# Performance work log

Measured on AMD Instinct MI355X. Metric: run time of the kernel, lower is better.

Reference implementation:

```python
import jax, jax.numpy as jnp
import numpy as np

N, E, ND, ED, H, OUT, L, VC = 10000, 160000, 8, 4, 128, 256, 6, 6
HEADS, C = 4, 128  # GATConv: out_channels=128 per head, concat=False -> mean over heads


def _ln(x, g, b, eps=1e-5):
    m = x.mean(-1, keepdims=True)
    v = ((x - m) ** 2).mean(-1, keepdims=True)
    return (x - m) * jax.lax.rsqrt(v + eps) * g + b


def _gat_layer(h, src, dst, e_attr, lw, a_src, a_dst, lew, a_edge, bias):
    # h: [N,H]; e_attr: [Etot,H]; PyG GATConv(heads=4, concat=False, edge_dim=H)
    xh = (h @ lw).reshape(N, HEADS, C)                 # [N,4,128]
    eh = (e_attr @ lew).reshape(-1, HEADS, C)          # [Etot,4,128]
    al_s = jnp.einsum('nhc,hc->nh', xh, a_src)
    al_d = jnp.einsum('nhc,hc->nh', xh, a_dst)
    al_e = jnp.einsum('ehc,hc->eh', eh, a_edge)
    alpha = jax.nn.leaky_relu(al_s[src] + al_d[dst] + al_e, 0.2)  # [Etot,4]
    amax = jax.ops.segment_max(alpha, dst, num_segments=N)
    ex = jnp.exp(alpha - amax[dst])
    den = jax.ops.segment_sum(ex, dst, num_segments=N)
    w = ex / (den[dst] + 1e-16)
    out = jax.ops.segment_sum(xh[src] * w[..., None], dst, num_segments=N)  # [N,4,128]
    return out.mean(axis=1) + bias


def setup_inputs() -> dict:
    key = jax.random.key(0)
    ks = jax.random.split(key, 32)
    s = 0.05
    d = {
        'x': jax.random.normal(ks[0], (N, ND), jnp.float32),
        'edge_index': jax.random.randint(ks[1], (2, E), 0, N),
        'edge_attr': jax.random.uniform(ks[2], (E, ED), jnp.float32),
        'vnf_context': jax.random.normal(ks[3], (1, VC), jnp.float32),
        # node embedding
        'node_w': jax.random.normal(ks[4], (ND, H)) * s, 'node_b': jnp.zeros((H,)),
        # EdgeAttentionLayer
        'ea_proj_w': jax.random.normal(ks[5], (ED, H)) * s, 'ea_proj_b': jnp.zeros((H,)),
        'vnf_w': jax.random.normal(ks[6], (VC, H)) * s, 'vnf_b': jnp.zeros((H,)),
        'att1_w': jax.random.normal(ks[7], (2 * H, H)) * s, 'att1_b': jnp.zeros((H,)),
        'att2_w': jax.random.normal(ks[8], (H, H // 2)) * s, 'att2_b': jnp.zeros((H // 2,)),
        'att3_w': jax.random.normal(ks[9], (H // 2, 1)) * s, 'att3_b': jnp.zeros((1,)),
        # per-layer GATConv params (stacked over L layers)
        'gat_lin_w': jax.random.normal(ks[10], (L, H, HEADS * C)) * s,
        'gat_att_src': jax.random.normal(ks[11], (L, HEADS, C)) * s,
        'gat_att_dst': jax.random.normal(ks[12], (L, HEADS, C)) * s,
        'gat_lin_edge_w': jax.random.normal(ks[13], (L, H, HEADS * C)) * s,
        'gat_att_edge': jax.random.normal(ks[14], (L, HEADS, C)) * s,
        'gat_bias': jnp.zeros((L, C)),
        'ln_scale': jnp.ones((L, H)), 'ln_bias': jnp.zeros((L, H)),
        # output projection
        'out_w': jax.random.normal(ks[15], (H, OUT)) * s, 'out_b': jnp.zeros((OUT,)),
    }
    return d


def reference(x, edge_index, edge_attr, vnf_context, node_w, node_b, ea_proj_w, ea_proj_b,
              vnf_w, vnf_b, att1_w, att1_b, att2_w, att2_b, att3_w, att3_b,
              gat_lin_w, gat_att_src, gat_att_dst, gat_lin_edge_w, gat_att_edge, gat_bias,
              ln_scale, ln_bias, out_w, out_b):
    src, dst = edge_index[0], edge_index[1]
    h = x @ node_w + node_b                                   # [N,128]
    # EdgeAttentionLayer (eval mode, no network_state)
    ef = edge_attr @ ea_proj_w + ea_proj_b                    # [E,128]
    vnf = vnf_context @ vnf_w + vnf_b                         # [1,128]
    comb = jnp.concatenate([ef, jnp.broadcast_to(vnf, (E, H))], axis=-1)
    a = jax.nn.relu(comb @ att1_w + att1_b)
    a = jax.nn.relu(a @ att2_w + att2_b)
    e_gate = jax.nn.sigmoid(a @ att3_w + att3_b)              # [E,1]
    w_edge = ef * e_gate                                      # [E,128]
    # GATConv default add_self_loops=True, fill_value='mean'
    loop = jnp.arange(N)
    src2 = jnp.concatenate([src, loop])
    dst2 = jnp.concatenate([dst, loop])
    e2 = jnp.concatenate([w_edge, jnp.broadcast_to(w_edge.mean(0, keepdims=True), (N, H))], axis=0)
    for l in range(L):
        hc = _gat_layer(h, src2, dst2, e2, gat_lin_w[l], gat_att_src[l], gat_att_dst[l],
                        gat_lin_edge_w[l], gat_att_edge[l], gat_bias[l])
        h = _ln(h + jax.nn.relu(hc), ln_scale[l], ln_bias[l])
    return h @ out_w + out_b                                  # [N,256]
```

## Files before the change

### kernel.cpp

```cpp
#include <hip/hip_runtime.h>
#include <hip/hip_bf16.h>
#include <math.h>

#define Nn 10000
#define Ee 160000
#define ET 170000
#define LL 6

typedef short v8s __attribute__((ext_vector_type(8)));
typedef float v4f __attribute__((ext_vector_type(4)));
typedef float v2f __attribute__((ext_vector_type(2)));

__device__ __forceinline__ unsigned short f2bf(float v) {
    unsigned int b = __float_as_uint(v);
    b += 0x7fffu + ((b >> 16) & 1u);
    return (unsigned short)(b >> 16);
}
__device__ __forceinline__ float bflo(unsigned int u) { return __uint_as_float(u << 16); }
__device__ __forceinline__ float bfhi(unsigned int u) { return __uint_as_float(u & 0xffff0000u); }

__global__ void k_node_embed(const float* __restrict__ x, const float* __restrict__ nw,
                             const float* __restrict__ nb, float* __restrict__ h,
                             unsigned short* __restrict__ hb) {
    int idx = blockIdx.x * 256 + threadIdx.x;
    if (idx >= Nn * 128) return;
    int n = idx >> 7, c = idx & 127;
    const float* xr = x + (size_t)n * 8;
    float acc = nb[c];
#pragma unroll
    for (int k = 0; k < 8; k++) acc += xr[k] * nw[k * 128 + c];
    h[idx] = acc;
    hb[idx] = f2bf(acc);
}

__global__ void k_small(const float* __restrict__ vnfc, const float* __restrict__ vw,
                        const float* __restrict__ vb, const float* __restrict__ eab,
                        const float* __restrict__ a1w, const float* __restrict__ a1b,
                        const float* __restrict__ eaw, float* __restrict__ E1) {
    __shared__ float vr[128];
    __shared__ float sM1[512];
    __shared__ float sd1[128];
    int t = threadIdx.x;
    if (t < 128) {
        float a = vb[t];
#pragma unroll
        for (int k = 0; k < 6; k++) a += vnfc[k] * vw[k * 128 + t];
        vr[t] = a;
    }
    __syncthreads();
    if (t < 128) {
        float a = a1b[t];
        for (int k = 0; k < 128; k++) a += eab[k] * a1w[k * 128 + t];
        for (int k = 0; k < 128; k++) a += vr[k] * a1w[(128 + k) * 128 + t];
        sd1[t] = a;
    }
    {
        int r = t >> 7, j = t & 127;
        float a = 0.f;
        for (int k = 0; k < 128; k++) a += eaw[r * 128 + k] * a1w[k * 128 + j];
        sM1[r * 128 + j] = a;
    }
    __syncthreads();
    if (t < 128) {
        E1[t * 8 + 0] = sM1[t];
        E1[t * 8 + 1] = sM1[128 + t];
        E1[t * 8 + 2] = sM1[256 + t];
        E1[t * 8 + 3] = sM1[384 + t];
        E1[t * 8 + 4] = sd1[t];
        E1[t * 8 + 5] = 0.f; E1[t * 8 + 6] = 0.f; E1[t * 8 + 7] = 0.f;
    }
}

__global__ void k_bmat(const float* __restrict__ glw, const float* __restrict__ gas,
                       const float* __restrict__ gad, const float* __restrict__ glew,
                       const float* __restrict__ gae, float* __restrict__ Bs,
                       float* __restrict__ Bd, float* __restrict__ Be) {
    int idx = blockIdx.x * 256 + threadIdx.x;
    if (idx >= LL * 128 * 4) return;
    int hh = idx & 3, k = (idx >> 2) & 127, l = idx >> 9;
    const float* lwp = glw  + (size_t)l * 65536 + k * 512 + hh * 128;
    const float* lep = glew + (size_t)l * 65536 + k * 512 + hh * 128;
    const float* sp = gas + l * 512 + hh * 128;
    const float* dp = gad + l * 512 + hh * 128;
    const float* ep = gae + l * 512 + hh * 128;
    float s1 = 0, s2 = 0, s3 = 0;
    for (int c = 0; c < 128; c++) {
        float lv = lwp[c];
        s1 += lv * sp[c];
        s2 += lv * dp[c];
        s3 += lep[c] * ep[c];
    }
    Bs[idx] = s1; Bd[idx] = s2; Be[idx] = s3;
}

__global__ void k_wsum(const float* __restrict__ glw, unsigned short* __restrict__ WsumT) {
    int idx = blockIdx.x * 256 + threadIdx.x;
    if (idx >= LL * 128 * 512) return;
    int kk = idx & 511;
    int c = (idx >> 9) & 127;
    int l = idx >> 16;
    float v = 0.25f * glw[(size_t)l * 65536 + (size_t)(kk & 127) * 512 + (kk >> 7) * 128 + c];
    WsumT[(size_t)l * 65536 + (size_t)c * 512 + kk] = f2bf(v);
}

__global__ void k_pb(const float* __restrict__ eaw, const float* __restrict__ eab,
                     const float* __restrict__ Be, float* __restrict__ PB,
                     float* __restrict__ cB) {
    int t = threadIdx.x;
    if (t >= 24) return;
    int l = t >> 2, hh = t & 3;
    const float* bp = Be + l * 512 + hh;
    float s0 = 0, s1 = 0, s2 = 0, s3 = 0, sc = 0;
    for (int k = 0; k < 128; k++) {
        float bv = bp[k * 4];
        s0 += eaw[0 * 128 + k] * bv;
        s1 += eaw[1 * 128 + k] * bv;
        s2 += eaw[2 * 128 + k] * bv;
        s3 += eaw[3 * 128 + k] * bv;
        sc += eab[k] * bv;
    }
    PB[0 * 24 + t] = s0; PB[1 * 24 + t] = s1;
    PB[2 * 24 + t] = s2; PB[3 * 24 + t] = s3;
    cB[t] = sc;
}

__global__ __launch_bounds__(256, 3) void k_edge(
    const float* __restrict__ ea, const float* __restrict__ E1,
    const float* __restrict__ a2w, const float* __restrict__ a2b,
    const float* __restrict__ a3w, const float* __restrict__ a3b,
    float* __restrict__ Gg, float4* __restrict__ Ge4, float* __restrict__ gsum) {
    __shared__ float sw2[128 * 64];
    __shared__ float4 sM[128];
    __shared__ float sD[128];
    __shared__ float prs[4][256];
    __shared__ float gsh[256];
    int t = threadIdx.x;
    int lane = t & 63;
    int p = t >> 6;
    int ps = __builtin_amdgcn_readfirstlane(p);
    for (int z = t; z < 2048; z += 256) ((float4*)sw2)[z] = ((const float4*)a2w)[z];
    if (t < 128) { sM[t] = *(const float4*)(E1 + t * 8); sD[t] = E1[t * 8 + 4]; }
    __syncthreads();
    int eb = blockIdx.x * 256 + lane;
    float4 ev[4];
#pragma unroll
    for (int r = 0; r < 4; r++) ev[r] = *(const float4*)(ea + (size_t)(eb + r * 64) * 4);
    v2f acc[4][8];
#pragma unroll
    for (int j = 0; j < 8; j++) {
        v2f b = {a2b[ps * 16 + 2 * j], a2b[ps * 16 + 2 * j + 1]};
#pragma unroll
        for (int r = 0; r < 4; r++) acc[r][j] = b;
    }
    const float* w2base = sw2 + ps * 16;
    for (int k = 0; k < 128; k++) {
        float4 m = sM[k];
        float dk = sD[k];
        v2f xx[4];
#pragma unroll
        for (int r = 0; r < 4; r++) {
            float xv = fmaxf(dk + ev[r].x * m.x + ev[r].y * m.y + ev[r].z * m.z + ev[r].w * m.w, 0.f);
            xx[r][0] = xv; xx[r][1] = xv;
        }
        const float* w2r = w2base + k * 64;
#pragma unroll
        for (int j4 = 0; j4 < 4; j4++) {
            float4 wv = *(const float4*)(w2r + j4 * 4);
            v2f w01 = {wv.x, wv.y}, w23 = {wv.z, wv.w};
#pragma unroll
            for (int r = 0; r < 4; r++) {
                acc[r][2 * j4]     += xx[r] * w01;
                acc[r][2 * j4 + 1] += xx[r] * w23;
            }
        }
    }
#pragma unroll
    for (int r = 0; r < 4; r++) {
        float pr = 0.f;
#pragma unroll
        for (int j = 0; j < 8; j++) {
            pr += fmaxf(acc[r][j][0], 0.f) * a3w[ps * 16 + 2 * j];
            pr += fmaxf(acc[r][j][1], 0.f) * a3w[ps * 16 + 2 * j + 1];
        }
        prs[p][r * 64 + lane] = pr;
    }
    __syncthreads();
    if (p == 0) {
        float v0 = 0.f, v1 = 0.f, v2 = 0.f, v3 = 0.f, v4 = 0.f;
#pragma unroll
        for (int rep = 0; rep < 4; rep++) {
            int le = rep * 64 + lane;
            float tot = prs[0][le] + prs[1][le] + prs[2][le] + prs[3][le] + a3b[0];
            float g = 1.f / (1.f + __expf(-tot));
            gsh[le] = g;
            float4 evv = ev[rep];
            v0 += g; v1 += g * evv.x; v2 += g * evv.y; v3 += g * evv.z; v4 += g * evv.w;
        }
#pragma unroll
        for (int d = 32; d > 0; d >>= 1) {
            v0 += __shfl_down(v0, d); v1 += __shfl_down(v1, d); v2 += __shfl_down(v2, d);
            v3 += __shfl_down(v3, d); v4 += __shfl_down(v4, d);
        }
        if (lane == 0) {
            atomicAdd(&gsum[0], v0); atomicAdd(&gsum[1], v1); atomicAdd(&gsum[2], v2);
            atomicAdd(&gsum[3], v3); atomicAdd(&gsum[4], v4);
        }
    }
    __syncthreads();
    {
        int e = blockIdx.x * 256 + ps * 64 + lane;
        float g = gsh[ps * 64 + lane];
        float4 evv = *(const float4*)(ea + (size_t)e * 4);
        Gg[e] = g;
        Ge4[e] = make_float4(g * evv.x, g * evv.y, g * evv.z, g * evv.w);
    }
}

__global__ void k_hist(const int* __restrict__ ei, int* __restrict__ hist) {
    int i = blockIdx.x * 256 + threadIdx.x;
    if (i >= ET) return;
    int d = (i < Ee) ? ei[Ee + i] : (i - Ee);
    atomicAdd(&hist[d], 1);
}

__global__ __launch_bounds__(1024) void k_scan(const int* __restrict__ hist,
                                               int* __restrict__ seg, int* __restrict__ pos) {
    __shared__ int wsums[16];
    __shared__ int carry_s;
    int t = threadIdx.x;
    int lane = t & 63, wid = t >> 6;
    if (t == 0) { carry_s = 0; seg[0] = 0; }
    __syncthreads();
    for (int base = 0; base < Nn; base += 1024) {
        int idx = base + t;
        int v = (idx < Nn) ? hist[idx] : 0;
        int sc = v;
#pragma unroll
        for (int d = 1; d < 64; d <<= 1) {
            int up = __shfl_up(sc, d);
            if (lane >= d) sc += up;
        }
        if (lane == 63) wsums[wid] = sc;
        __syncthreads();
        if (wid == 0) {
            int wv = (lane < 16) ? wsums[lane] : 0;
            int wsc = wv;
#pragma unroll
            for (int d = 1; d < 16; d <<= 1) {
                int up = __shfl_up(wsc, d);
                if (lane >= d) wsc += up;
            }
            if (lane < 16) wsums[lane] = wsc - wv;
        }
        __syncthreads();
        int carry = carry_s;
        int inc = sc + wsums[wid] + carry;
        if (idx < Nn) { seg[idx + 1] = inc; pos[idx] = inc - v; }
        __syncthreads();
        if (t == 1023) carry_s = inc;
        __syncthreads();
    }
}

__global__ void k_scatter(const int* __restrict__ ei, int* __restrict__ pos,
                          int2* __restrict__ pse) {
    int i = blockIdx.x * 256 + threadIdx.x;
    if (i >= ET) return;
    int s, d;
    if (i < Ee) { s = ei[i]; d = ei[Ee + i]; } else { s = d = i - Ee; }
    int idx = atomicAdd(&pos[d], 1);
    pse[idx] = make_int2(s, i);
}

__global__ void k_ales(const int2* __restrict__ pse, const float* __restrict__ Gg,
                       const float4* __restrict__ Ge4, const float* __restrict__ gsum,
                       const float* __restrict__ PB, const float* __restrict__ cB,
                       float4* __restrict__ aleS) {
    int i = blockIdx.x * 256 + threadIdx.x;
    if (i >= ET) return;
    int y = pse[i].y;
    float g;
    float4 ge;
    if (y < Ee) { g = Gg[y]; ge = Ge4[y]; }
    else {
        float inv = 1.f / Ee;
        g = gsum[0] * inv;
        ge = make_float4(gsum[1] * inv, gsum[2] * inv, gsum[3] * inv, gsum[4] * inv);
    }
#pragma unroll
    for (int l = 0; l < LL; l++) {
        float4 o;
        o.x = g * cB[l * 4 + 0] + ge.x * PB[0 * 24 + l * 4 + 0] + ge.y * PB[1 * 24 + l * 4 + 0]
            + ge.z * PB[2 * 24 + l * 4 + 0] + ge.w * PB[3 * 24 + l * 4 + 0];
        o.y = g * cB[l * 4 + 1] + ge.x * PB[0 * 24 + l * 4 + 1] + ge.y * PB[1 * 24 + l * 4 + 1]
            + ge.z * PB[2 * 24 + l * 4 + 1] + ge.w * PB[3 * 24 + l * 4 + 1];
        o.z = g * cB[l * 4 + 2] + ge.x * PB[0 * 24 + l * 4 + 2] + ge.y * PB[1 * 24 + l * 4 + 2]
            + ge.z * PB[2 * 24 + l * 4 + 2] + ge.w * PB[3 * 24 + l * 4 + 2];
        o.w = g * cB[l * 4 + 3] + ge.x * PB[0 * 24 + l * 4 + 3] + ge.y * PB[1 * 24 + l * 4 + 3]
            + ge.z * PB[2 * 24 + l * 4 + 3] + ge.w * PB[3 * 24 + l * 4 + 3];
        aleS[(size_t)l * ET + i] = o;
    }
}

__global__ void k_ab(const float* __restrict__ h, const float* __restrict__ Bs_l,
                     const float* __restrict__ Bd_l, float* __restrict__ als,
                     float* __restrict__ ald) {
    int idx = blockIdx.x * 256 + threadIdx.x;
    if (idx >= Nn * 8) return;
    int n = idx >> 3, slot = idx & 7;
    const float* B = (slot < 4) ? Bs_l : Bd_l;
    int hh = slot & 3;
    const float4* hr = (const float4*)(h + (size_t)n * 128);
    float s = 0.f;
#pragma unroll 8
    for (int kb = 0; kb < 32; kb++) {
        float4 hv = hr[kb];
        s += hv.x * B[(4 * kb + 0) * 4 + hh] + hv.y * B[(4 * kb + 1) * 4 + hh]
           + hv.z * B[(4 * kb + 2) * 4 + hh] + hv.w * B[(4 * kb + 3) * 4 + hh];
    }
    if (slot < 4) als[n * 4 + hh] = s;
    else          ald[n * 4 + hh] = s;
}

__global__ __launch_bounds__(256) void k_agg4(
    const int2* __restrict__ pse, const int* __restrict__ seg,
    const float* __restrict__ als, const float* __restrict__ ald,
    const float4* __restrict__ aleS_l, const unsigned short* __restrict__ hb,
    unsigned short* __restrict__ aggb) {
    __shared__ float part[3][512];
    __shared__ float pden[3][4];
    int t = threadIdx.x;
    int lane = t & 63;
    int wv = t >> 6;
    int n = blockIdx.x;
    int start = seg[n], end = seg[n + 1];
    int deg = end - start;
    int quarter = (deg + 3) >> 2;
    int s0 = start + wv * quarter;
    int e0 = min(s0 + quarter, end);
    int hp = lane >> 4;
    int cch = (lane & 15) * 8;
    float aldh = ald[n * 4 + hp];
    float den = 0.f;
    float4 acc0 = make_float4(0.f, 0.f, 0.f, 0.f);
    float4 acc1 = make_float4(0.f, 0.f, 0.f, 0.f);
    int i = s0;
    for (; i + 2 <= e0; i += 2) {
        int sa = pse[i].x, sb = pse[i + 1].x;
        float4 ala4 = aleS_l[i], alb4 = aleS_l[i + 1];
        float ala = hp == 0 ? ala4.x : hp == 1 ? ala4.y : hp == 2 ? ala4.z : ala4.w;
        float alb = hp == 0 ? alb4.x : hp == 1 ? alb4.y : hp == 2 ? alb4.z : alb4.w;
        float ava = als[sa * 4 + hp] + aldh + ala;
        float avb = als[sb * 4 + hp] + aldh + alb;
        ava = ava > 0.f ? ava : 0.2f * ava;
        avb = avb > 0.f ? avb : 0.2f * avb;
        float ea = __expf(fminf(ava, 60.f));
        float eb = __expf(fminf(avb, 60.f));
        den += ea + eb;
        uint4 ua = *(const uint4*)(hb + (size_t)sa * 128 + cch);
        uint4 ub = *(const uint4*)(hb + (size_t)sb * 128 + cch);
        acc0.x += ea * bflo(ua.x) + eb * bflo(ub.x);
        acc0.y += ea * bfhi(ua.x) + eb * bfhi(ub.x);
        acc0.z += ea * bflo(ua.y) + eb * bflo(ub.y);
        acc0.w += ea * bfhi(ua.y) + eb * bfhi(ub.y);
        acc1.x += ea * bflo(ua.z) + eb * bflo(ub.z);
        acc1.y += ea * bfhi(ua.z) + eb * bfhi(ub.z);
        acc1.z += ea * bflo(ua.w) + eb * bflo(ub.w);
        acc1.w += ea * bfhi(ua.w) + eb * bfhi(ub.w);
    }
    if (i < e0) {
        int sa = pse[i].x;
        float4 ala4 = aleS_l[i];
        float ala = hp == 0 ? ala4.x : hp == 1 ? ala4.y : hp == 2 ? ala4.z : ala4.w;
        float ava = als[sa * 4 + hp] + aldh + ala;
        ava = ava > 0.f ? ava : 0.2f * ava;
        float ea = __expf(fminf(ava, 60.f));
        den += ea;
        uint4 ua = *(const uint4*)(hb + (size_t)sa * 128 + cch);
        acc0.x += ea * bflo(ua.x); acc0.y += ea * bfhi(ua.x);
        acc0.z += ea * bflo(ua.y); acc0.w += ea * bfhi(ua.y);
        acc1.x += ea * bflo(ua.z); acc1.y += ea * bfhi(ua.z);
        acc1.z += ea * bflo(ua.w); acc1.w += ea * bfhi(ua.w);
    }
    if (wv > 0) {
        *(float4*)&part[wv - 1][lane * 8] = acc0;
        *(float4*)&part[wv - 1][lane * 8 + 4] = acc1;
        if ((lane & 15) == 0) pden[wv - 1][hp] = den;
    }
    __syncthreads();
    if (wv == 0) {
        float dtot = den + pden[0][hp] + pden[1][hp] + pden[2][hp];
#pragma unroll
        for (int r = 0; r < 3; r++) {
            float4 p0 = *(const float4*)&part[r][lane * 8];
            float4 p1 = *(const float4*)&part[r][lane * 8 + 4];
            acc0.x += p0.x; acc0.y += p0.y; acc0.z += p0.z; acc0.w += p0.w;
            acc1.x += p1.x; acc1.y += p1.y; acc1.z += p1.z; acc1.w += p1.w;
        }
        float inv = 1.f / (dtot + 1e-16f);
        acc0.x *= inv; acc0.y *= inv; acc0.z *= inv; acc0.w *= inv;
        acc1.x *= inv; acc1.y *= inv; acc1.z *= inv; acc1.w *= inv;
        ushort4 q0, q1;
        q0.x = f2bf(acc0.x); q0.y = f2bf(acc0.y); q0.z = f2bf(acc0.z); q0.w = f2bf(acc0.w);
        q1.x = f2bf(acc1.x); q1.y = f2bf(acc1.y); q1.z = f2bf(acc1.z); q1.w = f2bf(acc1.w);
        *(ushort4*)(aggb + (size_t)n * 512 + lane * 8) = q0;
        *(ushort4*)(aggb + (size_t)n * 512 + lane * 8 + 4) = q1;
    }
}

__global__ __launch_bounds__(256) void k_post(
    const unsigned short* __restrict__ aggb, const unsigned short* __restrict__ WsumT_l,
    const float* __restrict__ gbias, const float* __restrict__ lnsc,
    const float* __restrict__ lnbi, float* __restrict__ h,
    unsigned short* __restrict__ hb, const float* __restrict__ Bs_n,
    const float* __restrict__ Bd_n, float* __restrict__ als, float* __restrict__ ald) {
    int t = threadIdx.x;
    int lane = t & 63, w = t >> 6;
    int n0 = (blockIdx.x * 4 + w) * 16;
    if (n0 >= Nn) return;
    int m = lane & 15, q = lane >> 4;
    v4f acc[8];
#pragma unroll
    for (int nt = 0; nt < 8; nt++) acc[nt] = (v4f){0.f, 0.f, 0.f, 0.f};
    const unsigned short* arow = aggb + (size_t)(n0 + m) * 512 + q * 8;
#pragma unroll 4
    for (int ks = 0; ks < 16; ks++) {
        v8s fa = *(const v8s*)(arow + ks * 32);
#pragma unroll
        for (int nt = 0; nt < 8; nt++) {
            int col = nt * 16 + m;
            v8s fb = *(const v8s*)(WsumT_l + (size_t)col * 512 + ks * 32 + q * 8);
            acc[nt] = __builtin_amdgcn_mfma_f32_16x16x32_bf16(fa, fb, acc[nt], 0, 0, 0);
        }
    }
    float v[8][4];
    float s1[4] = {0.f, 0.f, 0.f, 0.f}, s2[4] = {0.f, 0.f, 0.f, 0.f};
#pragma unroll
    for (int nt = 0; nt < 8; nt++) {
        int col = nt * 16 + m;
        float b = gbias[col];
#pragma unroll
        for (int r = 0; r < 4; r++) {
            int row = n0 + q * 4 + r;
            float val = h[(size_t)row * 128 + col] + fmaxf(acc[nt][r] + b, 0.f);
            v[nt][r] = val;
            s1[r] += val; s2[r] += val * val;
        }
    }
#pragma unroll
    for (int d = 1; d <= 8; d <<= 1) {
#pragma unroll
        for (int r = 0; r < 4; r++) {
            s1[r] += __shfl_xor(s1[r], d);
            s2[r] += __shfl_xor(s2[r], d);
        }
    }
    float o8[8][4];
#pragma unroll
    for (int r = 0; r < 4; r++) {
        float mean = s1[r] * (1.f / 128.f);
        float var = s2[r] * (1.f / 128.f) - mean * mean;
        float rinv = rsqrtf(var + 1e-5f);
        int row = n0 + q * 4 + r;
#pragma unroll
        for (int nt = 0; nt < 8; nt++) {
            int col = nt * 16 + m;
            float o = (v[nt][r] - mean) * rinv * lnsc[col] + lnbi[col];
            o8[nt][r] = o;
            h[(size_t)row * 128 + col] = o;
            hb[(size_t)row * 128 + col] = f2bf(o);
        }
    }
    float sal[4][4], sad[4][4];
#pragma unroll
    for (int r = 0; r < 4; r++) {
#pragma unroll
        for (int hh = 0; hh < 4; hh++) { sal[r][hh] = 0.f; sad[r][hh] = 0.f; }
    }
#pragma unroll
    for (int nt = 0; nt < 8; nt++) {
        int col = nt * 16 + m;
        float4 bs = *(const float4*)(Bs_n + col * 4);
        float4 bd = *(const float4*)(Bd_n + col * 4);
#pragma unroll
        for (int r = 0; r < 4; r++) {
            float o = o8[nt][r];
            sal[r][0] += o * bs.x; sal[r][1] += o * bs.y;
            sal[r][2] += o * bs.z; sal[r][3] += o * bs.w;
            sad[r][0] += o * bd.x; sad[r][1] += o * bd.y;
            sad[r][2] += o * bd.z; sad[r][3] += o * bd.w;
        }
    }
#pragma unroll
    for (int d = 1; d <= 8; d <<= 1) {
#pragma unroll
        for (int r = 0; r < 4; r++) {
#pragma unroll
            for (int hh = 0; hh < 4; hh++) {
                sal[r][hh] += __shfl_xor(sal[r][hh], d);
                sad[r][hh] += __shfl_xor(sad[r][hh], d);
            }
        }
    }
    if (m < 8) {
        int hh = m & 3;
#pragma unroll
        for (int r = 0; r < 4; r++) {
            int row = n0 + q * 4 + r;
            float va = (hh == 0) ? sal[r][0] : (hh == 1) ? sal[r][1] : (hh == 2) ? sal[r][2] : sal[r][3];
            float vd = (hh == 0) ? sad[r][0] : (hh == 1) ? sad[r][1] : (hh == 2) ? sad[r][2] : sad[r][3];
            if (m < 4) als[row * 4 + hh] = va;
            else       ald[row * 4 + hh] = vd;
        }
    }
}

__global__ __launch_bounds__(256) void k_out(
    const float* __restrict__ h, const float* __restrict__ ow,
    const float* __restrict__ ob, float* __restrict__ out) {
    __shared__ float4 hs4[8][32];
    int t = threadIdx.x;
    int n0 = blockIdx.x * 8;
    if (t < 256) {
        int i = t >> 5, kb = t & 31;
        hs4[i][kb] = *(const float4*)(h + (size_t)(n0 + i) * 128 + 4 * kb);
    }
    __syncthreads();
    float acc[8] = {0, 0, 0, 0, 0, 0, 0, 0};
    for (int kb = 0; kb < 32; kb++) {
        float w0 = ow[(4 * kb + 0) * 256 + t];
        float w1 = ow[(4 * kb + 1) * 256 + t];
        float w2 = ow[(4 * kb + 2) * 256 + t];
        float w3 = ow[(4 * kb + 3) * 256 + t];
#pragma unroll
        for (int i = 0; i < 8; i++) {
            float4 hv = hs4[i][kb];
            acc[i] += hv.x * w0 + hv.y * w1 + hv.z * w2 + hv.w * w3;
        }
    }
    float b = ob[t];
#pragma unroll
    for (int i = 0; i < 8; i++) out[(size_t)(n0 + i) * 256 + t] = acc[i] + b;
}

extern "C" void kernel_launch(void* const* d_in, const int* in_sizes, int n_in,
                              void* d_out, int out_size, void* d_ws, size_t ws_size,
                              hipStream_t stream) {
    const float* x    = (const float*)d_in[0];
    const int*   ei   = (const int*)d_in[1];
    const float* ea   = (const float*)d_in[2];
    const float* vnfc = (const float*)d_in[3];
    const float* nw   = (const float*)d_in[4];
    const float* nb   = (const float*)d_in[5];
    const float* eaw  = (const float*)d_in[6];
    const float* eab  = (const float*)d_in[7];
    const float* vw   = (const float*)d_in[8];
    const float* vb   = (const float*)d_in[9];
    const float* a1w  = (const float*)d_in[10];
    const float* a1b  = (const float*)d_in[11];
    const float* a2w  = (const float*)d_in[12];
    const float* a2b  = (const float*)d_in[13];
    const float* a3w  = (const float*)d_in[14];
    const float* a3b  = (const float*)d_in[15];
    const float* glw  = (const float*)d_in[16];
    const float* gas  = (const float*)d_in[17];
    const float* gad  = (const float*)d_in[18];
    const float* glew = (const float*)d_in[19];
    const float* gae  = (const float*)d_in[20];
    const float* gb   = (const float*)d_in[21];
    const float* lnsc = (const float*)d_in[22];
    const float* lnbi = (const float*)d_in[23];
    const float* ow   = (const float*)d_in[24];
    const float* ob   = (const float*)d_in[25];
    float* out = (float*)d_out;

    char* w = (char*)d_ws;
    size_t o = 0;
    auto allocf = [&](size_t cnt) { float* p = (float*)(w + o); o += ((cnt * 4 + 255) / 256) * 256; return p; };
    auto alloci = [&](size_t cnt) { int* p = (int*)(w + o); o += ((cnt * 4 + 255) / 256) * 256; return p; };
    auto allocu = [&](size_t cnt) { unsigned short* p = (unsigned short*)(w + o); o += ((cnt * 2 + 255) / 256) * 256; return p; };
    float* h      = allocf((size_t)Nn * 128);
    unsigned short* hb    = allocu((size_t)Nn * 128);
    unsigned short* aggb  = allocu((size_t)Nn * 512);
    unsigned short* WsumT = allocu((size_t)LL * 128 * 512);
    float* als    = allocf((size_t)Nn * 4);
    float* ald    = allocf((size_t)Nn * 4);
    float* Gg     = allocf((size_t)Ee);
    float4* Ge4   = (float4*)allocf((size_t)Ee * 4);
    float4* aleS  = (float4*)allocf((size_t)LL * ET * 4);
    float* Bs     = allocf(3072);
    float* Bd     = allocf(3072);
    float* Be     = allocf(3072);
    float* E1     = allocf(1024);
    float* PB     = allocf(96);
    float* cB     = allocf(24);
    float* gsum   = allocf(8);
    int* seg  = alloci(Nn + 1);
    int* hist = alloci(Nn);
    int* pos  = alloci(Nn);
    int2* pse = (int2*)alloci((size_t)ET * 2);

    hipMemsetAsync(hist, 0, Nn * sizeof(int), stream);
    hipMemsetAsync(gsum, 0, 8 * sizeof(float), stream);

    k_node_embed<<<(Nn * 128 + 255) / 256, 256, 0, stream>>>(x, nw, nb, h, hb);
    k_small<<<1, 512, 0, stream>>>(vnfc, vw, vb, eab, a1w, a1b, eaw, E1);
    k_bmat<<<(LL * 128 * 4 + 255) / 256, 256, 0, stream>>>(glw, gas, gad, glew, gae, Bs, Bd, Be);
    k_wsum<<<(LL * 128 * 512 + 255) / 256, 256, 0, stream>>>(glw, WsumT);
    k_pb<<<1, 32, 0, stream>>>(eaw, eab, Be, PB, cB);
    k_edge<<<Ee / 256, 256, 0, stream>>>(ea, E1, a2w, a2b, a3w, a3b, Gg, Ge4, gsum);
    k_hist<<<(ET + 255) / 256, 256, 0, stream>>>(ei, hist);
    k_scan<<<1, 1024, 0, stream>>>(hist, seg, pos);
    k_scatter<<<(ET + 255) / 256, 256, 0, stream>>>(ei, pos, pse);
    k_ales<<<(ET + 255) / 256, 256, 0, stream>>>(pse, Gg, Ge4, gsum, PB, cB, aleS);
    k_ab<<<(Nn * 8 + 255) / 256, 256, 0, stream>>>(h, Bs, Bd, als, ald);
    for (int l = 0; l < LL; l++) {
        int ln = (l + 1) % LL;
        k_agg4<<<Nn, 256, 0, stream>>>(pse, seg, als, ald, aleS + (size_t)l * ET, hb, aggb);
        k_post<<<(625 + 3) / 4, 256, 0, stream>>>(aggb, WsumT + (size_t)l * 65536,
                                                  gb + l * 128, lnsc + l * 128, lnbi + l * 128,
                                                  h, hb, Bs + ln * 512, Bd + ln * 512, als, ald);
    }
    k_out<<<Nn / 8, 256, 0, stream>>>(h, ow, ob, out);
}
```

Measured before the change: 564.2 us.

## Fuse per-layer GAT kernels and output projection into one cooperative persistent kernel

Replaces the 12 per-layer launches of the aggregation and post kernels, plus the final output kernel, with a single cooperative persistent kernel that uses grid-wide syncs between phases. The post phase is also redistributed so each 16-row tile is handled by a whole block, four waves with two column tiles each, and the layernorm and attention-logit reductions go through shared memory. The aim is to remove launch overhead and tail effects. In exchange it adds grid.sync costs and less parallelism per node: the aggregation now loops over nodes with a grid capped at 2048 blocks instead of launching 10000 blocks.

```diff
diff --git a/kernel.cpp b/kernel.cpp
--- a/kernel.cpp
+++ b/kernel.cpp
@@ -1,6 +1,9 @@
 #include <hip/hip_runtime.h>
+#include <hip/hip_cooperative_groups.h>
 #include <hip/hip_bf16.h>
 #include <math.h>
+
+namespace cg = cooperative_groups;
 
 #define Nn 10000
 #define Ee 160000
@@ -322,225 +325,260 @@
     else          ald[n * 4 + hh] = s;
 }
 
-__global__ __launch_bounds__(256) void k_agg4(
+__global__ __launch_bounds__(256) void k_loop(
     const int2* __restrict__ pse, const int* __restrict__ seg,
-    const float* __restrict__ als, const float* __restrict__ ald,
-    const float4* __restrict__ aleS_l, const unsigned short* __restrict__ hb,
-    unsigned short* __restrict__ aggb) {
-    __shared__ float part[3][512];
-    __shared__ float pden[3][4];
+    float* __restrict__ als, float* __restrict__ ald,
+    const float4* __restrict__ aleS, unsigned short* __restrict__ hb,
+    unsigned short* __restrict__ aggb, const unsigned short* __restrict__ WsumT,
+    const float* __restrict__ gball, const float* __restrict__ lnscall,
+    const float* __restrict__ lnbiall, float* __restrict__ h,
+    const float* __restrict__ Bs, const float* __restrict__ Bd,
+    const float* __restrict__ ow, const float* __restrict__ ob,
+    float* __restrict__ out) {
+    __shared__ float smem[1664];
+    cg::grid_group grid = cg::this_grid();
     int t = threadIdx.x;
     int lane = t & 63;
-    int wv = t >> 6;
-    int n = blockIdx.x;
-    int start = seg[n], end = seg[n + 1];
-    int deg = end - start;
-    int quarter = (deg + 3) >> 2;
-    int s0 = start + wv * quarter;
-    int e0 = min(s0 + quarter, end);
-    int hp = lane >> 4;
-    int cch = (lane & 15) * 8;
-    float aldh = ald[n * 4 + hp];
-    float den = 0.f;
-    float4 acc0 = make_float4(0.f, 0.f, 0.f, 0.f);
-    float4 acc1 = make_float4(0.f, 0.f, 0.f, 0.f);
-    int i = s0;
-    for (; i + 2 <= e0; i += 2) {
-        int sa = pse[i].x, sb = pse[i + 1].x;
-        float4 ala4 = aleS_l[i], alb4 = aleS_l[i + 1];
-        float ala = hp == 0 ? ala4.x : hp == 1 ? ala4.y : hp == 2 ? ala4.z : ala4.w;
-        float alb = hp == 0 ? alb4.x : hp == 1 ? alb4.y : hp == 2 ? alb4.z : alb4.w;
-        float ava = als[sa * 4 + hp] + aldh + ala;
-        float avb = als[sb * 4 + hp] + aldh + alb;
-        ava = ava > 0.f ? ava : 0.2f * ava;
-        avb = avb > 0.f ? avb : 0.2f * avb;
-        float ea = __expf(fminf(ava, 60.f));
-        float eb = __expf(fminf(avb, 60.f));
-        den += ea + eb;
-        uint4 ua = *(const uint4*)(hb + (size_t)sa * 128 + cch);
-        uint4 ub = *(const uint4*)(hb + (size_t)sb * 128 + cch);
-        acc0.x += ea * bflo(ua.x) + eb * bflo(ub.x);
-        acc0.y += ea * bfhi(ua.x) + eb * bfhi(ub.x);
-        acc0.z += ea * bflo(ua.y) + eb * bflo(ub.y);
-        acc0.w += ea * bfhi(ua.y) + eb * bfhi(ub.y);
-        acc1.x += ea * bflo(ua.z) + eb * bflo(ub.z);
-        acc1.y += ea * bfhi(ua.z) + eb * bfhi(ub.z);
-        acc1.z += ea * bflo(ua.w) + eb * bflo(ub.w);
-        acc1.w += ea * bfhi(ua.w) + eb * bfhi(ub.w);
-    }
-    if (i < e0) {
-        int sa = pse[i].x;
-        float4 ala4 = aleS_l[i];
-        float ala = hp == 0 ? ala4.x : hp == 1 ? ala4.y : hp == 2 ? ala4.z : ala4.w;
-        float ava = als[sa * 4 + hp] + aldh + ala;
-        ava = ava > 0.f ? ava : 0.2f * ava;
-        float ea = __expf(fminf(ava, 60.f));
-        den += ea;
-        uint4 ua = *(const uint4*)(hb + (size_t)sa * 128 + cch);
-        acc0.x += ea * bflo(ua.x); acc0.y += ea * bfhi(ua.x);
-        acc0.z += ea * bflo(ua.y); acc0.w += ea * bfhi(ua.y);
-        acc1.x += ea * bflo(ua.z); acc1.y += ea * bfhi(ua.z);
-        acc1.z += ea * bflo(ua.w); acc1.w += ea * bfhi(ua.w);
-    }
-    if (wv > 0) {
-        *(float4*)&part[wv - 1][lane * 8] = acc0;
-        *(float4*)&part[wv - 1][lane * 8 + 4] = acc1;
-        if ((lane & 15) == 0) pden[wv - 1][hp] = den;
-    }
-    __syncthreads();
-    if (wv == 0) {
-        float dtot = den + pden[0][hp] + pden[1][hp] + pden[2][hp];
-#pragma unroll
-        for (int r = 0; r < 3; r++) {
-            float4 p0 = *(const float4*)&part[r][lane * 8];
-            float4 p1 = *(const float4*)&part[r][lane * 8 + 4];
-            acc0.x += p0.x; acc0.y += p0.y; acc0.z += p0.z; acc0.w += p0.w;
-            acc1.x += p1.x; acc1.y += p1.y; acc1.z += p1.z; acc1.w += p1.w;
-        }
-        float inv = 1.f / (dtot + 1e-16f);
-        acc0.x *= inv; acc0.y *= inv; acc0.z *= inv; acc0.w *= inv;
-        acc1.x *= inv; acc1.y *= inv; acc1.z *= inv; acc1.w *= inv;
-        ushort4 q0, q1;
-        q0.x = f2bf(acc0.x); q0.y = f2bf(acc0.y); q0.z = f2bf(acc0.z); q0.w = f2bf(acc0.w);
-        q1.x = f2bf(acc1.x); q1.y = f2bf(acc1.y); q1.z = f2bf(acc1.z); q1.w = f2bf(acc1.w);
-        *(ushort4*)(aggb + (size_t)n * 512 + lane * 8) = q0;
-        *(ushort4*)(aggb + (size_t)n * 512 + lane * 8 + 4) = q1;
-    }
-}
-
-__global__ __launch_bounds__(256) void k_post(
-    const unsigned short* __restrict__ aggb, const unsigned short* __restrict__ WsumT_l,
-    const float* __restrict__ gbias, const float* __restrict__ lnsc,
-    const float* __restrict__ lnbi, float* __restrict__ h,
-    unsigned short* __restrict__ hb, const float* __restrict__ Bs_n,
-    const float* __restrict__ Bd_n, float* __restrict__ als, float* __restrict__ ald) {
-    int t = threadIdx.x;
-    int lane = t & 63, w = t >> 6;
-    int n0 = (blockIdx.x * 4 + w) * 16;
-    if (n0 >= Nn) return;
-    int m = lane & 15, q = lane >> 4;
-    v4f acc[8];
-#pragma unroll
-    for (int nt = 0; nt < 8; nt++) acc[nt] = (v4f){0.f, 0.f, 0.f, 0.f};
-    const unsigned short* arow = aggb + (size_t)(n0 + m) * 512 + q * 8;
+    int w4 = t >> 6;
+    for (int l = 0; l < LL; l++) {
+        const float4* aleS_l = aleS + (size_t)l * ET;
+        float* part = smem;
+        float* pden = smem + 1536;
+        for (int n = blockIdx.x; n < Nn; n += gridDim.x) {
+            int start = seg[n], end = seg[n + 1];
+            int deg = end - start;
+            int quarter = (deg + 3) >> 2;
+            int s0 = start + w4 * quarter;
+            int e0 = min(s0 + quarter, end);
+            int hp = lane >> 4;
+            int cch = (lane & 15) * 8;
+            float aldh = ald[n * 4 + hp];
+            float den = 0.f;
+            float4 acc0 = make_float4(0.f, 0.f, 0.f, 0.f);
+            float4 acc1 = make_float4(0.f, 0.f, 0.f, 0.f);
+            int i = s0;
+            for (; i + 2 <= e0; i += 2) {
+                int sa = pse[i].x, sb = pse[i + 1].x;
+                float4 ala4 = aleS_l[i], alb4 = aleS_l[i + 1];
+                float ala = hp == 0 ? ala4.x : hp == 1 ? ala4.y : hp == 2 ? ala4.z : ala4.w;
+                float alb = hp == 0 ? alb4.x : hp == 1 ? alb4.y : hp == 2 ? alb4.z : alb4.w;
+                float ava = als[sa * 4 + hp] + aldh + ala;
+                float avb = als[sb * 4 + hp] + aldh + alb;
+                ava = ava > 0.f ? ava : 0.2f * ava;
+                avb = avb > 0.f ? avb : 0.2f * avb;
+                float ea = __expf(fminf(ava, 60.f));
+                float eb = __expf(fminf(avb, 60.f));
+                den += ea + eb;
+                uint4 ua = *(const uint4*)(hb + (size_t)sa * 128 + cch);
+                uint4 ub = *(const uint4*)(hb + (size_t)sb * 128 + cch);
+                acc0.x += ea * bflo(ua.x) + eb * bflo(ub.x);
+                acc0.y += ea * bfhi(ua.x) + eb * bfhi(ub.x);
+                acc0.z += ea * bflo(ua.y) + eb * bflo(ub.y);
+                acc0.w += ea * bfhi(ua.y) + eb * bfhi(ub.y);
+                acc1.x += ea * bflo(ua.z) + eb * bflo(ub.z);
+                acc1.y += ea * bfhi(ua.z) + eb * bfhi(ub.z);
+                acc1.z += ea * bflo(ua.w) + eb * bflo(ub.w);
+                acc1.w += ea * bfhi(ua.w) + eb * bfhi(ub.w);
+            }
+            if (i < e0) {
+                int sa = pse[i].x;
+                float4 ala4 = aleS_l[i];
+                float ala = hp == 0 ? ala4.x : hp == 1 ? ala4.y : hp == 2 ? ala4.z : ala4.w;
+                float ava = als[sa * 4 + hp] + aldh + ala;
+                ava = ava > 0.f ? ava : 0.2f * ava;
+                float ea = __expf(fminf(ava, 60.f));
+                den += ea;
+                uint4 ua = *(const uint4*)(hb + (size_t)sa * 128 + cch);
+                acc0.x += ea * bflo(ua.x); acc0.y += ea * bfhi(ua.x);
+                acc0.z += ea * bflo(ua.y); acc0.w += ea * bfhi(ua.y);
+                acc1.x += ea * bflo(ua.z); acc1.y += ea * bfhi(ua.z);
+                acc1.z += ea * bflo(ua.w); acc1.w += ea * bfhi(ua.w);
+            }
+            if (w4 > 0) {
+                *(float4*)&part[(w4 - 1) * 512 + lane * 8] = acc0;
+                *(float4*)&part[(w4 - 1) * 512 + lane * 8 + 4] = acc1;
+                if ((lane & 15) == 0) pden[(w4 - 1) * 4 + hp] = den;
+            }
+            __syncthreads();
+            if (w4 == 0) {
+                float dtot = den + pden[0 * 4 + hp] + pden[1 * 4 + hp] + pden[2 * 4 + hp];
+#pragma unroll
+                for (int r = 0; r < 3; r++) {
+                    float4 p0 = *(const float4*)&part[r * 512 + lane * 8];
+                    float4 p1 = *(const float4*)&part[r * 512 + lane * 8 + 4];
+                    acc0.x += p0.x; acc0.y += p0.y; acc0.z += p0.z; acc0.w += p0.w;
+                    acc1.x += p1.x; acc1.y += p1.y; acc1.z += p1.z; acc1.w += p1.w;
+                }
+                float inv = 1.f / (dtot + 1e-16f);
+                acc0.x *= inv; acc0.y *= inv; acc0.z *= inv; acc0.w *= inv;
+                acc1.x *= inv; acc1.y *= inv; acc1.z *= inv; acc1.w *= inv;
+                ushort4 q0, q1;
+                q0.x = f2bf(acc0.x); q0.y = f2bf(acc0.y); q0.z = f2bf(acc0.z); q0.w = f2bf(acc0.w);
+                q1.x = f2bf(acc1.x); q1.y = f2bf(acc1.y); q1.z = f2bf(acc1.z); q1.w = f2bf(acc1.w);
+                *(ushort4*)(aggb + (size_t)n * 512 + lane * 8) = q0;
+                *(ushort4*)(aggb + (size_t)n * 512 + lane * 8 + 4) = q1;
+            }
+            __syncthreads();
+        }
+        __threadfence();
+        grid.sync();
+        const unsigned short* W_l = WsumT + (size_t)l * 65536;
+        const float* gbias = gball + l * 128;
+        const float* ls = lnscall + l * 128;
+        const float* lb = lnbiall + l * 128;
+        int ln = (l + 1) % LL;
+        const float* Bs_n = Bs + ln * 512;
+        const float* Bd_n = Bd + ln * 512;
+        float* sred1 = smem;
+        float* sred2 = smem + 64;
+        float* sA    = smem + 128;
+        float* sDd   = smem + 384;
+        for (int tile = blockIdx.x; tile < Nn / 16; tile += gridDim.x) {
+            int n0 = tile * 16;
+            int m = lane & 15, q = lane >> 4;
+            v4f accv[2];
+            accv[0] = (v4f){0.f, 0.f, 0.f, 0.f};
+            accv[1] = (v4f){0.f, 0.f, 0.f, 0.f};
+            const unsigned short* arow = aggb + (size_t)(n0 + m) * 512 + q * 8;
+            int col0 = (2 * w4) * 16 + m, col1 = col0 + 16;
 #pragma unroll 4
-    for (int ks = 0; ks < 16; ks++) {
-        v8s fa = *(const v8s*)(arow + ks * 32);
-#pragma unroll
-        for (int nt = 0; nt < 8; nt++) {
-            int col = nt * 16 + m;
-            v8s fb = *(const v8s*)(WsumT_l + (size_t)col * 512 + ks * 32 + q * 8);
-            acc[nt] = __builtin_amdgcn_mfma_f32_16x16x32_bf16(fa, fb, acc[nt], 0, 0, 0);
-        }
-    }
-    float v[8][4];
-    float s1[4] = {0.f, 0.f, 0.f, 0.f}, s2[4] = {0.f, 0.f, 0.f, 0.f};
-#pragma unroll
-    for (int nt = 0; nt < 8; nt++) {
-        int col = nt * 16 + m;
-        float b = gbias[col];
-#pragma unroll
-        for (int r = 0; r < 4; r++) {
-            int row = n0 + q * 4 + r;
-            float val = h[(size_t)row * 128 + col] + fmaxf(acc[nt][r] + b, 0.f);
-            v[nt][r] = val;
-            s1[r] += val; s2[r] += val * val;
-        }
-    }
-#pragma unroll
-    for (int d = 1; d <= 8; d <<= 1) {
-#pragma unroll
-        for (int r = 0; r < 4; r++) {
-            s1[r] += __shfl_xor(s1[r], d);
-            s2[r] += __shfl_xor(s2[r], d);
-        }
-    }
-    float o8[8][4];
-#pragma unroll
-    for (int r = 0; r < 4; r++) {
-        float mean = s1[r] * (1.f / 128.f);
-        float var = s2[r] * (1.f / 128.f) - mean * mean;
-        float rinv = rsqrtf(var + 1e-5f);
-        int row = n0 + q * 4 + r;
-#pragma unroll
-        for (int nt = 0; nt < 8; nt++) {
-            int col = nt * 16 + m;
-            float o = (v[nt][r] - mean) * rinv * lnsc[col] + lnbi[col];
-            o8[nt][r] = o;
-            h[(size_t)row * 128 + col] = o;
-            hb[(size_t)row * 128 + col] = f2bf(o);
-        }
-    }
-    float sal[4][4], sad[4][4];
-#pragma unroll
-    for (int r = 0; r < 4; r++) {
-#pragma unroll
-        for (int hh = 0; hh < 4; hh++) { sal[r][hh] = 0.f; sad[r][hh] = 0.f; }
-    }
-#pragma unroll
-    for (int nt = 0; nt < 8; nt++) {
-        int col = nt * 16 + m;
-        float4 bs = *(const float4*)(Bs_n + col * 4);
-        float4 bd = *(const float4*)(Bd_n + col * 4);
-#pragma unroll
-        for (int r = 0; r < 4; r++) {
-            float o = o8[nt][r];
-            sal[r][0] += o * bs.x; sal[r][1] += o * bs.y;
-            sal[r][2] += o * bs.z; sal[r][3] += o * bs.w;
-            sad[r][0] += o * bd.x; sad[r][1] += o * bd.y;
-            sad[r][2] += o * bd.z; sad[r][3] += o * bd.w;
-        }
-    }
-#pragma unroll
-    for (int d = 1; d <= 8; d <<= 1) {
-#pragma unroll
-        for (int r = 0; r < 4; r++) {
-#pragma unroll
-            for (int hh = 0; hh < 4; hh++) {
-                sal[r][hh] += __shfl_xor(sal[r][hh], d);
-                sad[r][hh] += __shfl_xor(sad[r][hh], d);
-            }
-        }
-    }
-    if (m < 8) {
-        int hh = m & 3;
-#pragma unroll
-        for (int r = 0; r < 4; r++) {
-            int row = n0 + q * 4 + r;
-            float va = (hh == 0) ? sal[r][0] : (hh == 1) ? sal[r][1] : (hh == 2) ? sal[r][2] : sal[r][3];
-            float vd = (hh == 0) ? sad[r][0] : (hh == 1) ? sad[r][1] : (hh == 2) ? sad[r][2] : sad[r][3];
-            if (m < 4) als[row * 4 + hh] = va;
-            else       ald[row * 4 + hh] = vd;
-        }
-    }
-}
-
-__global__ __launch_bounds__(256) void k_out(
-    const float* __restrict__ h, const float* __restrict__ ow,
-    const float* __restrict__ ob, float* __restrict__ out) {
-    __shared__ float4 hs4[8][32];
-    int t = threadIdx.x;
-    int n0 = blockIdx.x * 8;
-    if (t < 256) {
-        int i = t >> 5, kb = t & 31;
-        hs4[i][kb] = *(const float4*)(h + (size_t)(n0 + i) * 128 + 4 * kb);
-    }
-    __syncthreads();
-    float acc[8] = {0, 0, 0, 0, 0, 0, 0, 0};
-    for (int kb = 0; kb < 32; kb++) {
-        float w0 = ow[(4 * kb + 0) * 256 + t];
-        float w1 = ow[(4 * kb + 1) * 256 + t];
-        float w2 = ow[(4 * kb + 2) * 256 + t];
-        float w3 = ow[(4 * kb + 3) * 256 + t];
-#pragma unroll
-        for (int i = 0; i < 8; i++) {
-            float4 hv = hs4[i][kb];
-            acc[i] += hv.x * w0 + hv.y * w1 + hv.z * w2 + hv.w * w3;
-        }
-    }
-    float b = ob[t];
-#pragma unroll
-    for (int i = 0; i < 8; i++) out[(size_t)(n0 + i) * 256 + t] = acc[i] + b;
+            for (int ks = 0; ks < 16; ks++) {
+                v8s fa = *(const v8s*)(arow + ks * 32);
+                v8s fb0 = *(const v8s*)(W_l + (size_t)col0 * 512 + ks * 32 + q * 8);
+                v8s fb1 = *(const v8s*)(W_l + (size_t)col1 * 512 + ks * 32 + q * 8);
+                accv[0] = __builtin_amdgcn_mfma_f32_16x16x32_bf16(fa, fb0, accv[0], 0, 0, 0);
+                accv[1] = __builtin_amdgcn_mfma_f32_16x16x32_bf16(fa, fb1, accv[1], 0, 0, 0);
+            }
+            float v[2][4];
+            float s1[4] = {0.f, 0.f, 0.f, 0.f}, s2[4] = {0.f, 0.f, 0.f, 0.f};
+#pragma unroll
+            for (int j = 0; j < 2; j++) {
+                int col = j == 0 ? col0 : col1;
+                float b = gbias[col];
+#pragma unroll
+                for (int r = 0; r < 4; r++) {
+                    int row = n0 + q * 4 + r;
+                    float val = h[(size_t)row * 128 + col] + fmaxf(accv[j][r] + b, 0.f);
+                    v[j][r] = val;
+                    s1[r] += val; s2[r] += val * val;
+                }
+            }
+#pragma unroll
+            for (int d = 1; d <= 8; d <<= 1) {
+#pragma unroll
+                for (int r = 0; r < 4; r++) {
+                    s1[r] += __shfl_xor(s1[r], d);
+                    s2[r] += __shfl_xor(s2[r], d);
+                }
+            }
+            if (m == 0) {
+#pragma unroll
+                for (int r = 0; r < 4; r++) {
+                    sred1[w4 * 16 + q * 4 + r] = s1[r];
+                    sred2[w4 * 16 + q * 4 + r] = s2[r];
+                }
+            }
+            __syncthreads();
+            float o2[2][4];
+#pragma unroll
+            for (int r = 0; r < 4; r++) {
+                int row = q * 4 + r;
+                float t1 = sred1[row] + sred1[16 + row] + sred1[32 + row] + sred1[48 + row];
+                float t2 = sred2[row] + sred2[16 + row] + sred2[32 + row] + sred2[48 + row];
+                float mean = t1 * (1.f / 128.f);
+                float var = t2 * (1.f / 128.f) - mean * mean;
+                float rinv = rsqrtf(var + 1e-5f);
+                int grow = n0 + row;
+#pragma unroll
+                for (int j = 0; j < 2; j++) {
+                    int col = j == 0 ? col0 : col1;
+                    float o = (v[j][r] - mean) * rinv * ls[col] + lb[col];
+                    o2[j][r] = o;
+                    h[(size_t)grow * 128 + col] = o;
+                    hb[(size_t)grow * 128 + col] = f2bf(o);
+                }
+            }
+            float sal[4][4], sad[4][4];
+#pragma unroll
+            for (int r = 0; r < 4; r++)
+#pragma unroll
+                for (int hh = 0; hh < 4; hh++) { sal[r][hh] = 0.f; sad[r][hh] = 0.f; }
+#pragma unroll
+            for (int j = 0; j < 2; j++) {
+                int col = j == 0 ? col0 : col1;
+                float4 bs = *(const float4*)(Bs_n + col * 4);
+                float4 bd = *(const float4*)(Bd_n + col * 4);
+#pragma unroll
+                for (int r = 0; r < 4; r++) {
+                    float o = o2[j][r];
+                    sal[r][0] += o * bs.x; sal[r][1] += o * bs.y;
+                    sal[r][2] += o * bs.z; sal[r][3] += o * bs.w;
+                    sad[r][0] += o * bd.x; sad[r][1] += o * bd.y;
+                    sad[r][2] += o * bd.z; sad[r][3] += o * bd.w;
+                }
+            }
+#pragma unroll
+            for (int d = 1; d <= 8; d <<= 1) {
+#pragma unroll
+                for (int r = 0; r < 4; r++)
+#pragma unroll
+                    for (int hh = 0; hh < 4; hh++) {
+                        sal[r][hh] += __shfl_xor(sal[r][hh], d);
+                        sad[r][hh] += __shfl_xor(sad[r][hh], d);
+                    }
+            }
+            if (m == 0) {
+#pragma unroll
+                for (int r = 0; r < 4; r++)
+#pragma unroll
+                    for (int hh = 0; hh < 4; hh++) {
+                        sA[w4 * 64 + (q * 4 + r) * 4 + hh] = sal[r][hh];
+                        sDd[w4 * 64 + (q * 4 + r) * 4 + hh] = sad[r][hh];
+                    }
+            }
+            __syncthreads();
+            if (t < 128) {
+                int row = t >> 3, slot = t & 7, hh = slot & 3;
+                if (slot < 4) {
+                    float va = sA[row * 4 + hh] + sA[64 + row * 4 + hh]
+                             + sA[128 + row * 4 + hh] + sA[192 + row * 4 + hh];
+                    als[(n0 + row) * 4 + hh] = va;
+                } else {
+                    float vd = sDd[row * 4 + hh] + sDd[64 + row * 4 + hh]
+                             + sDd[128 + row * 4 + hh] + sDd[192 + row * 4 + hh];
+                    ald[(n0 + row) * 4 + hh] = vd;
+                }
+            }
+            __syncthreads();
+        }
+        __threadfence();
+        grid.sync();
+    }
+    float4* hs4 = (float4*)smem;
+    for (int tile = blockIdx.x; tile < Nn / 8; tile += gridDim.x) {
+        int n0 = tile * 8;
+        {
+            int i = t >> 5, kb = t & 31;
+            hs4[i * 32 + kb] = *(const float4*)(h + (size_t)(n0 + i) * 128 + 4 * kb);
+        }
+        __syncthreads();
+        float acc[8] = {0, 0, 0, 0, 0, 0, 0, 0};
+        for (int kb = 0; kb < 32; kb++) {
+            float w0 = ow[(4 * kb + 0) * 256 + t];
+            float w1 = ow[(4 * kb + 1) * 256 + t];
+            float w2 = ow[(4 * kb + 2) * 256 + t];
+            float w3 = ow[(4 * kb + 3) * 256 + t];
+#pragma unroll
+            for (int i = 0; i < 8; i++) {
+                float4 hv = hs4[i * 32 + kb];
+                acc[i] += hv.x * w0 + hv.y * w1 + hv.z * w2 + hv.w * w3;
+            }
+        }
+        float b = ob[t];
+#pragma unroll
+        for (int i = 0; i < 8; i++) out[(size_t)(n0 + i) * 256 + t] = acc[i] + b;
+        __syncthreads();
+    }
 }
 
 extern "C" void kernel_launch(void* const* d_in, const int* in_sizes, int n_in,
@@ -614,12 +652,19 @@
     k_scatter<<<(ET + 255) / 256, 256, 0, stream>>>(ei, pos, pse);
     k_ales<<<(ET + 255) / 256, 256, 0, stream>>>(pse, Gg, Ge4, gsum, PB, cB, aleS);
     k_ab<<<(Nn * 8 + 255) / 256, 256, 0, stream>>>(h, Bs, Bd, als, ald);
-    for (int l = 0; l < LL; l++) {
-        int ln = (l + 1) % LL;
-        k_agg4<<<Nn, 256, 0, stream>>>(pse, seg, als, ald, aleS + (size_t)l * ET, hb, aggb);
-        k_post<<<(625 + 3) / 4, 256, 0, stream>>>(aggb, WsumT + (size_t)l * 65536,
-                                                  gb + l * 128, lnsc + l * 128, lnbi + l * 128,
-                                                  h, hb, Bs + ln * 512, Bd + ln * 512, als, ald);
-    }
-    k_out<<<Nn / 8, 256, 0, stream>>>(h, ow, ob, out);
-}
+
+    int nbpc = 0;
+    hipOccupancyMaxActiveBlocksPerMultiprocessor(&nbpc, k_loop, 256, 0);
+    if (nbpc < 1) nbpc = 1;
+    int grid = nbpc * 256;
+    if (grid > 2048) grid = 2048;
+    const int2* pse_c = pse;
+    const float4* aleS_c = aleS;
+    const unsigned short* WsumT_c = WsumT;
+    const int* seg_c = seg;
+    void* args[] = {(void*)&pse_c, (void*)&seg_c, (void*)&als, (void*)&ald,
+                    (void*)&aleS_c, (void*)&hb, (void*)&aggb, (void*)&WsumT_c,
+                    (void*)&gb, (void*)&lnsc, (void*)&lnbi, (void*)&h,
+                    (void*)&Bs, (void*)&Bd, (void*)&ow, (void*)&ob, (void*)&out};
+    hipLaunchCooperativeKernel((const void*)k_loop, dim3(grid), dim3(256), args, 0, stream);
+}
```

Measured after the change: 1.595 ms. 2.83x slower.
